# Optimization experiments

Hardware: AMD Instinct MI355X
Metric: run time of the kernel (lower is better)

## Reference

```python
import jax, jax.numpy as jnp
import numpy as np

N = 100000
E = 600000
D = 128
H = 8
DH = D // H
T = 32
NET = 2


def _ln(x, g, b, eps=1e-5):
    mu = jnp.mean(x, axis=-1, keepdims=True)
    var = jnp.mean((x - mu) ** 2, axis=-1, keepdims=True)
    return (x - mu) * jax.lax.rsqrt(var + eps) * g + b


def _expmap(e, c):
    abs_c = jnp.maximum(jnp.abs(c), 1e-15)
    sq = jnp.sqrt(abs_c)
    n = jnp.maximum(jnp.linalg.norm(e, axis=-1, keepdims=True), 1e-15)
    tanh_p = jnp.tanh(sq * n) * e / (sq * n)
    tan_p = jnp.tan(sq * n) * e / (sq * n)
    return jnp.where(c < 0, tanh_p, tan_p)


def _proj(x, c, eps=1e-5):
    abs_c = jnp.maximum(jnp.abs(c), 1e-15)
    maxnorm = (1.0 - eps) / jnp.sqrt(abs_c)
    norm = jnp.linalg.norm(x, axis=-1, keepdims=True)
    scale = jnp.where(norm > maxnorm, maxnorm / norm, jnp.ones_like(norm))
    return x * scale


def _forward(x, time_emb, edge_time, Wq, Wk, Wv, rel_q, rel_k, rel_v, Wt, bt,
             Wd1, bd1, Wd2, bd2, decay_scale, c_mag, hyp_beta, logit_alpha,
             Wo, bo, g1, be1, g2, be2, Wf1, bf1, Wf2, bf2, src, dst, edge_type):
    n = x.shape[0]
    Q = (x @ Wq).reshape(n, H, DH)
    K = (x @ Wk).reshape(n, H, DH)
    V = (x @ Wv).reshape(n, H, DH)
    # per-edge gathers + relation embeddings
    q_dst = Q[dst] + rel_q[edge_type].reshape(-1, H, DH)
    k_src = K[src] + rel_k[edge_type].reshape(-1, H, DH)
    v_src = V[src] + rel_v[edge_type].reshape(-1, H, DH)
    k_src = k_src + (time_emb @ Wt + bt).reshape(-1, H, DH)
    euclid = jnp.sum(q_dst * k_src, axis=-1) / np.float32(np.sqrt(DH))  # (E,H)
    # decay MLP: input = [edge_time, normalized edge_type]
    denom_t = jnp.maximum(1.0, edge_type.max().astype(jnp.float32) + 1.0)
    et = edge_type.astype(jnp.float32)[:, None] / denom_t
    dec_in = jnp.concatenate([edge_time[:, None], et], axis=-1)  # (E,2)
    decay_raw = jnp.tanh(jax.nn.relu(dec_in @ Wd1 + bd1) @ Wd2 + bd2)  # (E,H)
    decay = jnp.exp(decay_scale[None, :] * decay_raw)
    euclid = euclid * decay
    # hyperbolic branch
    c = -jnp.abs(c_mag)
    m = _proj(_expmap(x, c), c)
    man_dist = jnp.linalg.norm(m[src] - m[dst], axis=-1)[:, None]  # (E,1)
    hyp = -hyp_beta[None, :] * man_dist * decay
    alpha = jax.nn.sigmoid(logit_alpha)[None, :]
    logits = alpha * euclid + (1.0 - alpha) * hyp  # (E,H)
    # scatter softmax over incoming edges of each dst node
    seg_max = jax.ops.segment_max(logits, dst, num_segments=n)
    ex = jnp.exp(logits - seg_max[dst])
    denom = jax.ops.segment_sum(ex, dst, num_segments=n)
    attn = ex / denom[dst]
    agg = jax.ops.segment_sum(v_src * attn[..., None], dst, num_segments=n).reshape(n, D)
    out = agg @ Wo + bo
    x = _ln(x + out, g1, be1)
    ffn = jax.nn.gelu(x @ Wf1 + bf1, approximate=False) @ Wf2 + bf2
    x = _ln(x + ffn, g2, be2)
    return x


def setup_inputs() -> dict:
    key = jax.random.key(0)
    ks = jax.random.split(key, 20)

    def lin(k, fi, fo):
        return jax.random.normal(k, (fi, fo), jnp.float32) / np.float32(np.sqrt(fi))

    return {
        "x": jax.random.normal(ks[0], (N, D), jnp.float32),
        "edge_index": jax.random.randint(ks[1], (2, E), 0, N),
        "time_emb": jax.random.normal(ks[2], (E, T), jnp.float32),
        "edge_type": jax.random.randint(ks[3], (E,), 0, NET),
        "edge_time": jax.random.uniform(ks[4], (E,), jnp.float32),
        "Wq": lin(ks[5], D, D), "Wk": lin(ks[6], D, D), "Wv": lin(ks[7], D, D),
        "rel_q": jax.random.normal(ks[8], (NET, D), jnp.float32) * 0.1,
        "rel_k": jax.random.normal(ks[9], (NET, D), jnp.float32) * 0.1,
        "rel_v": jax.random.normal(ks[10], (NET, D), jnp.float32) * 0.1,
        "Wt": lin(ks[11], T, D), "bt": jnp.zeros((D,), jnp.float32),
        "Wd1": lin(ks[12], 2, 64), "bd1": jnp.zeros((64,), jnp.float32),
        "Wd2": lin(ks[13], 64, H), "bd2": jnp.zeros((H,), jnp.float32),
        "decay_scale": jnp.full((H,), 0.5, jnp.float32),
        "c_mag": jnp.asarray(1.0, jnp.float32),
        "hyp_beta": jnp.ones((H,), jnp.float32),
        "logit_alpha": jnp.zeros((H,), jnp.float32),
        "Wo": lin(ks[14], D, D), "bo": jnp.zeros((D,), jnp.float32),
        "g1": jnp.ones((D,), jnp.float32), "be1": jnp.zeros((D,), jnp.float32),
        "g2": jnp.ones((D,), jnp.float32), "be2": jnp.zeros((D,), jnp.float32),
        "Wf1": lin(ks[15], D, 4 * D), "bf1": jnp.zeros((4 * D,), jnp.float32),
        "Wf2": lin(ks[16], 4 * D, D), "bf2": jnp.zeros((D,), jnp.float32),
    }


def reference(x, edge_index, time_emb, edge_type, edge_time, Wq, Wk, Wv,
              rel_q, rel_k, rel_v, Wt, bt, Wd1, bd1, Wd2, bd2, decay_scale,
              c_mag, hyp_beta, logit_alpha, Wo, bo, g1, be1, g2, be2,
              Wf1, bf1, Wf2, bf2):
    src, dst = edge_index[0], edge_index[1]
    return _forward(x, time_emb, edge_time, Wq, Wk, Wv, rel_q, rel_k, rel_v,
                    Wt, bt, Wd1, bd1, Wd2, bd2, decay_scale, c_mag, hyp_beta,
                    logit_alpha, Wo, bo, g1, be1, g2, be2, Wf1, bf1, Wf2, bf2,
                    src, dst, edge_type)
```

## Files before the change

kernel.cpp:

```cpp
#include <hip/hip_runtime.h>

constexpr int NN = 100000;
constexpr int EE = 600000;
constexpr int DD = 128;
constexpr int HH = 8;
constexpr int NB = (NN + 255) / 256;

constexpr long long OFF_Q    = 0;
constexpr long long OFF_K    = OFF_Q    + (long long)NN*DD;
constexpr long long OFF_V    = OFF_K    + (long long)NN*DD;
constexpr long long OFF_LOG  = OFF_V    + (long long)NN*DD;
constexpr long long OFF_T    = OFF_LOG  + (long long)EE*HH;
constexpr long long OFF_U    = OFF_T    + (long long)NN;
constexpr long long OFF_ETM  = OFF_U    + (long long)NN;
constexpr long long OFF_CNT  = OFF_ETM  + 4;
constexpr long long OFF_CUR  = OFF_CNT  + (long long)NN;
constexpr long long OFF_RP   = OFF_CUR  + (long long)NN;
constexpr long long OFF_ES   = OFF_RP   + (long long)NN + 4;
constexpr long long OFF_SRCS = OFF_ES   + (long long)EE;
constexpr long long OFF_DSTS = OFF_SRCS + (long long)EE;
constexpr long long OFF_ETS  = OFF_DSTS + (long long)EE;
constexpr long long OFF_BS   = OFF_ETS  + (long long)EE;

typedef float f32x4 __attribute__((ext_vector_type(4)));
typedef short s16x8 __attribute__((ext_vector_type(8)));

__device__ inline float gelu_exact(float v) {
    return 0.5f * v * (1.0f + erff(v * 0.70710678118654752440f));
}
__device__ inline void bsplit1(float x, unsigned short& hb, unsigned short& lb) {
    unsigned u = __float_as_uint(x);
    hb = (unsigned short)(u >> 16);
    float rem = x - __uint_as_float(((unsigned)hb) << 16);
    lb = (unsigned short)(__float_as_uint(rem) >> 16);
}

__global__ __launch_bounds__(256) void k_zero(int* __restrict__ cnt, int* __restrict__ cur,
                                              int* __restrict__ etmax) {
    int stride = gridDim.x * 256;
    for (int i = blockIdx.x * 256 + threadIdx.x; i < NN; i += stride) { cnt[i] = 0; cur[i] = 0; }
    if (blockIdx.x == 0 && threadIdx.x == 0) etmax[0] = 0;
}

__global__ __launch_bounds__(256) void k_etmax(const int* __restrict__ etype, int* __restrict__ etmax) {
    int lmax = 0;
    int stride = gridDim.x * 256;
    for (int i = blockIdx.x * 256 + threadIdx.x; i < EE; i += stride) lmax = max(lmax, etype[i]);
    for (int m = 1; m < 64; m <<= 1) lmax = max(lmax, __shfl_xor(lmax, m));
    if ((threadIdx.x & 63) == 0) atomicMax(etmax, lmax);
}

__global__ __launch_bounds__(256) void k_hist(const int* __restrict__ eidx, int* __restrict__ cnt) {
    int i = blockIdx.x * 256 + threadIdx.x;
    if (i < EE) atomicAdd(&cnt[eidx[EE + i]], 1);
}
__global__ __launch_bounds__(256) void k_scan1(const int* __restrict__ cnt, int* __restrict__ bs) {
    __shared__ int wsum[4];
    int i = blockIdx.x * 256 + threadIdx.x;
    int v = (i < NN) ? cnt[i] : 0;
    for (int m = 1; m < 64; m <<= 1) v += __shfl_xor(v, m);
    if ((threadIdx.x & 63) == 0) wsum[threadIdx.x >> 6] = v;
    __syncthreads();
    if (threadIdx.x == 0) bs[blockIdx.x] = wsum[0] + wsum[1] + wsum[2] + wsum[3];
}
__global__ __launch_bounds__(512) void k_scan2(int* __restrict__ bs) {
    __shared__ int s[512];
    int t = threadIdx.x;
    int v = (t < NB) ? bs[t] : 0;
    s[t] = v;
    __syncthreads();
    for (int off = 1; off < 512; off <<= 1) {
        int val = 0;
        if (t >= off) val = s[t - off];
        __syncthreads();
        if (t >= off) s[t] += val;
        __syncthreads();
    }
    if (t < NB) bs[t] = s[t] - v;
}
__global__ __launch_bounds__(256) void k_scan3(const int* __restrict__ cnt, const int* __restrict__ bs,
                                               int* __restrict__ rp) {
    __shared__ int s[256];
    int t = threadIdx.x;
    int i = blockIdx.x * 256 + t;
    int v = (i < NN) ? cnt[i] : 0;
    s[t] = v;
    __syncthreads();
    for (int off = 1; off < 256; off <<= 1) {
        int val = 0;
        if (t >= off) val = s[t - off];
        __syncthreads();
        if (t >= off) s[t] += val;
        __syncthreads();
    }
    int incl = s[t];
    int off0 = bs[blockIdx.x];
    if (i < NN) rp[i] = off0 + incl - v;
    if (i == NN - 1) rp[NN] = off0 + incl;
}
__global__ __launch_bounds__(256) void k_scatter(const int* __restrict__ eidx, const int* __restrict__ etype,
                                                 const int* __restrict__ rp, int* __restrict__ cur,
                                                 int* __restrict__ es, int* __restrict__ src_s,
                                                 int* __restrict__ dst_s, int* __restrict__ et_s) {
    int i = blockIdx.x * 256 + threadIdx.x;
    if (i < EE) {
        int d = eidx[EE + i];
        int pos = rp[d] + atomicAdd(&cur[d], 1);
        es[pos] = i;
        src_s[pos] = eidx[i];
        dst_s[pos] = d;
        et_s[pos] = etype[i];
    }
}

__global__ __launch_bounds__(256) void k_qkv(const float* __restrict__ x,
                                             const float* __restrict__ Wq, const float* __restrict__ Wk,
                                             const float* __restrict__ Wv,
                                             float* __restrict__ Q, float* __restrict__ K, float* __restrict__ V) {
    __shared__ float Ast[32][72];
    __shared__ float Bs[32][72];
    int tid = threadIdx.x;
    int nt = blockIdx.y;
    int mat = nt >> 1;
    int colbase = (nt & 1) * 64;
    const float* W = (mat == 0) ? Wq : (mat == 1) ? Wk : Wv;
    float* Out = (mat == 0) ? Q : (mat == 1) ? K : V;
    int row0 = blockIdx.x * 64;
    int tx = tid & 15, ty = tid >> 4;
    float acc[4][4] = {};
    for (int k0 = 0; k0 < 128; k0 += 32) {
        {
            int r = tid >> 3;
            int c = (tid & 7) * 4;
            #pragma unroll
            for (int rr = 0; rr < 2; ++rr) {
                int lrow = r + rr * 32;
                int grow = row0 + lrow;
                float4 v = make_float4(0.f, 0.f, 0.f, 0.f);
                if (grow < NN) v = *(const float4*)&x[(long long)grow * 128 + k0 + c];
                Ast[c + 0][lrow] = v.x; Ast[c + 1][lrow] = v.y;
                Ast[c + 2][lrow] = v.z; Ast[c + 3][lrow] = v.w;
            }
            int kk = tid >> 4;
            int cc = (tid & 15) * 4;
            #pragma unroll
            for (int k2 = 0; k2 < 2; ++k2) {
                int kr = kk + k2 * 16;
                *(float4*)&Bs[kr][cc] = *(const float4*)&W[(k0 + kr) * 128 + colbase + cc];
            }
        }
        __syncthreads();
        #pragma unroll
        for (int kk = 0; kk < 32; ++kk) {
            float4 a = *(const float4*)&Ast[kk][ty * 4];
            float4 b = *(const float4*)&Bs[kk][tx * 4];
            float av[4] = {a.x, a.y, a.z, a.w};
            float bv[4] = {b.x, b.y, b.z, b.w};
            #pragma unroll
            for (int i = 0; i < 4; ++i)
                #pragma unroll
                for (int j = 0; j < 4; ++j) acc[i][j] += av[i] * bv[j];
        }
        __syncthreads();
    }
    #pragma unroll
    for (int i = 0; i < 4; ++i) {
        int grow = row0 + ty * 4 + i;
        if (grow < NN)
            *(float4*)&Out[(long long)grow * 128 + colbase + tx * 4] =
                make_float4(acc[i][0], acc[i][1], acc[i][2], acc[i][3]);
    }
}

__global__ __launch_bounds__(256) void k_tu(const float* __restrict__ x, const float* __restrict__ c_mag,
                                            float* __restrict__ T, float* __restrict__ U) {
    int wid = threadIdx.x >> 6;
    int lane = threadIdx.x & 63;
    int row = blockIdx.x * 4 + wid;
    if (row >= NN) return;
    float c = -fabsf(c_mag[0]);
    float abs_c = fmaxf(fabsf(c), 1e-15f);
    float sq = sqrtf(abs_c);
    float2 xv = *(const float2*)&x[(long long)row * 128 + lane * 2];
    float s = xv.x * xv.x + xv.y * xv.y;
    for (int m = 1; m < 64; m <<= 1) s += __shfl_xor(s, m);
    float nt = sqrtf(s);
    float n = fmaxf(nt, 1e-15f);
    float arg = sq * n;
    float f = ((c < 0.0f) ? tanhf(arg) : tanf(arg)) / arg;
    float norm = fabsf(f) * nt;
    float maxnorm = (1.0f - 1e-5f) / sq;
    float scale = (norm > maxnorm) ? (maxnorm / norm) : 1.0f;
    float t = f * scale;
    if (lane == 0) { T[row] = t; U[row] = t * t * s; }
}

__global__ __launch_bounds__(256) void k_logits(const float* __restrict__ Q, const float* __restrict__ K,
                                                const float* __restrict__ x, const float* __restrict__ T,
                                                const float* __restrict__ U, const float* __restrict__ temb,
                                                const int* __restrict__ es, const int* __restrict__ src_s,
                                                const int* __restrict__ dst_s, const int* __restrict__ et_s,
                                                const float* __restrict__ etime,
                                                const float* __restrict__ rel_q, const float* __restrict__ rel_k,
                                                const float* __restrict__ Wt, const float* __restrict__ bt,
                                                const float* __restrict__ Wd1, const float* __restrict__ bd1,
                                                const float* __restrict__ Wd2, const float* __restrict__ bd2,
                                                const float* __restrict__ dscale, const int* __restrict__ etmax,
                                                const float* __restrict__ hyp_beta,
                                                const float* __restrict__ logit_alpha,
                                                float* __restrict__ LOG) {
    __shared__ float Ts[32][32];
    __shared__ float TP[32][128];
    __shared__ float Dec[32][8];
    __shared__ float Wd1s[128];
    __shared__ float bd1s[64];
    __shared__ float Wd2s[512];
    int tid = threadIdx.x;
    int pb0 = blockIdx.x * 32;
    {
        int er = tid >> 3;
        int c = (tid & 7) * 4;
        int e = es[pb0 + er];
        *(float4*)&Ts[er][c] = *(const float4*)&temb[(long long)e * 32 + c];
        if (tid < 128) Wd1s[tid] = Wd1[tid];
        if (tid >= 128 && tid < 192) bd1s[tid - 128] = bd1[tid - 128];
        Wd2s[tid] = Wd2[tid];
        Wd2s[tid + 256] = Wd2[tid + 256];
    }
    __syncthreads();
    {
        int el = tid >> 3, hh = tid & 7;
        int pos = pb0 + el;
        float denom_t = fmaxf(1.0f, (float)(etmax[0]) + 1.0f);
        float in0 = etime[es[pos]];
        float in1 = (float)et_s[pos] / denom_t;
        float acc = bd2[hh];
        #pragma unroll
        for (int j = 0; j < 64; ++j) {
            float hid = fmaxf(in0 * Wd1s[j] + in1 * Wd1s[64 + j] + bd1s[j], 0.0f);
            acc += hid * Wd2s[j * 8 + hh];
        }
        Dec[el][hh] = expf(dscale[hh] * tanhf(acc));
    }
    {
        int c4 = (tid & 31) * 4;
        int g = tid >> 5;
        float4 bt4 = *(const float4*)&bt[c4];
        float4 a0 = bt4, a1 = bt4, a2 = bt4, a3 = bt4;
        for (int t = 0; t < 32; ++t) {
            float4 w = *(const float4*)&Wt[t * 128 + c4];
            float f0 = Ts[g][t], f1 = Ts[g + 8][t], f2 = Ts[g + 16][t], f3 = Ts[g + 24][t];
            a0.x += f0 * w.x; a0.y += f0 * w.y; a0.z += f0 * w.z; a0.w += f0 * w.w;
            a1.x += f1 * w.x; a1.y += f1 * w.y; a1.z += f1 * w.z; a1.w += f1 * w.w;
            a2.x += f2 * w.x; a2.y += f2 * w.y; a2.z += f2 * w.z; a2.w += f2 * w.w;
            a3.x += f3 * w.x; a3.y += f3 * w.y; a3.z += f3 * w.z; a3.w += f3 * w.w;
        }
        *(float4*)&TP[g][c4] = a0;
        *(float4*)&TP[g + 8][c4] = a1;
        *(float4*)&TP[g + 16][c4] = a2;
        *(float4*)&TP[g + 24][c4] = a3;
    }
    __syncthreads();
    int wid = tid >> 6;
    int lane = tid & 63;
    int half = lane >> 5;
    int l = lane & 31;
    int d4 = l * 4;
    int h = l >> 2;
    float alpha = 1.0f / (1.0f + expf(-logit_alpha[h]));
    float beta = hyp_beta[h];
    #pragma unroll
    for (int i = 0; i < 4; ++i) {
        int elocal = wid * 8 + i * 2 + half;
        int pos = pb0 + elocal;
        int src = src_s[pos], dst = dst_s[pos];
        int et = et_s[pos];
        float4 q  = *(const float4*)&Q[(long long)dst * 128 + d4];
        float4 rq = *(const float4*)&rel_q[et * 128 + d4];
        float4 k  = *(const float4*)&K[(long long)src * 128 + d4];
        float4 rk = *(const float4*)&rel_k[et * 128 + d4];
        float4 tp = *(const float4*)&TP[elocal][d4];
        float4 xs = *(const float4*)&x[(long long)src * 128 + d4];
        float4 xd = *(const float4*)&x[(long long)dst * 128 + d4];
        float ep = (q.x + rq.x) * (k.x + rk.x + tp.x)
                 + (q.y + rq.y) * (k.y + rk.y + tp.y)
                 + (q.z + rq.z) * (k.z + rk.z + tp.z)
                 + (q.w + rq.w) * (k.w + rk.w + tp.w);
        float dp = xs.x * xd.x + xs.y * xd.y + xs.z * xd.z + xs.w * xd.w;
        ep += __shfl_xor(ep, 1); ep += __shfl_xor(ep, 2);
        dp += __shfl_xor(dp, 1); dp += __shfl_xor(dp, 2); dp += __shfl_xor(dp, 4);
        dp += __shfl_xor(dp, 8); dp += __shfl_xor(dp, 16);
        float man2 = fmaxf(U[src] + U[dst] - 2.0f * T[src] * T[dst] * dp, 0.0f);
        float man = sqrtf(man2);
        float dec = Dec[elocal][h];
        float eu = ep * 0.25f * dec;
        float hyp = -beta * man * dec;
        float lg = alpha * eu + (1.0f - alpha) * hyp;
        if ((l & 3) == 0) LOG[(long long)pos * 8 + h] = lg;
    }
}

__global__ __launch_bounds__(256) void k_agg2(const int* __restrict__ rp, const int* __restrict__ src_s,
                                              const int* __restrict__ et_s,
                                              const float* __restrict__ V, const float* __restrict__ rel_v,
                                              const float* __restrict__ LOG, float* __restrict__ AGG) {
    int wid = threadIdx.x >> 6, lane = threadIdx.x & 63;
    int node = blockIdx.x * 4 + wid;
    if (node >= NN) return;
    int beg = rp[node], end = rp[node + 1];
    int d = lane * 2;
    int h = lane >> 3;
    float mx = -3.0e38f;
    for (int i = beg; i < end; ++i) {
        mx = fmaxf(mx, LOG[(long long)i * 8 + h]);
    }
    float den = 0.0f;
    float ax = 0.0f, ay = 0.0f;
    for (int i = beg; i < end; ++i) {
        int src = src_s[i];
        int et = et_s[i];
        float ex = expf(LOG[(long long)i * 8 + h] - mx);
        den += ex;
        float2 v  = *(const float2*)&V[(long long)src * 128 + d];
        float2 rv = *(const float2*)&rel_v[et * 128 + d];
        ax += (v.x + rv.x) * ex;
        ay += (v.y + rv.y) * ex;
    }
    float sc = (end > beg) ? (1.0f / den) : 0.0f;
    *(float2*)&AGG[(long long)node * 128 + d] = make_float2(ax * sc, ay * sc);
}

__global__ __launch_bounds__(256) void k_cvt(const float* __restrict__ Wf1, const float* __restrict__ Wf2,
                                             unsigned short* __restrict__ W1h, unsigned short* __restrict__ W1l,
                                             unsigned short* __restrict__ W2h, unsigned short* __restrict__ W2l) {
    int idx = blockIdx.x * 256 + threadIdx.x;
    {
        int tile = idx >> 11, rem = idx & 2047;
        int ks = rem >> 9, rem2 = rem & 511;
        int l = rem2 >> 3, j = rem2 & 7;
        int k = ks * 32 + ((l >> 4) << 3) + j;
        int n = (tile << 4) + (l & 15);
        unsigned short hb, lb;
        bsplit1(Wf1[k * 512 + n], hb, lb);
        W1h[idx] = hb; W1l[idx] = lb;
    }
    {
        int tile = idx >> 13;
        int ks = (idx >> 9) & 15;
        int l = (idx >> 3) & 63, j = idx & 7;
        int k = ks * 32 + ((l >> 4) << 3) + j;
        int n = (tile << 4) + (l & 15);
        unsigned short hb, lb;
        bsplit1(Wf2[k * 128 + n], hb, lb);
        W2h[idx] = hb; W2l[idx] = lb;
    }
}

__global__ __launch_bounds__(256) void k_out_ln1(float* AGGY1,
                                                 const float* __restrict__ Wo,
                                                 const float* __restrict__ bo, const float* __restrict__ x,
                                                 const float* __restrict__ g1, const float* __restrict__ be1) {
    __shared__ float Ast[32][40];
    __shared__ float Bs[32][136];
    int tid = threadIdx.x;
    int row0 = blockIdx.x * 32;
    int tx = tid & 31, ty = tid >> 5;
    float acc[4][4] = {};
    for (int k0 = 0; k0 < 128; k0 += 32) {
        {
            int r = tid >> 3, c = (tid & 7) * 4;
            float4 v = *(const float4*)&AGGY1[(long long)(row0 + r) * 128 + k0 + c];
            Ast[c + 0][r] = v.x; Ast[c + 1][r] = v.y; Ast[c + 2][r] = v.z; Ast[c + 3][r] = v.w;
            int kk = tid >> 5, cc = (tid & 31) * 4;
            #pragma unroll
            for (int k2 = 0; k2 < 4; ++k2) {
                int kr = kk + k2 * 8;
                *(float4*)&Bs[kr][cc] = *(const float4*)&Wo[(k0 + kr) * 128 + cc];
            }
        }
        __syncthreads();
        #pragma unroll
        for (int kk = 0; kk < 32; ++kk) {
            float4 a = *(const float4*)&Ast[kk][ty * 4];
            float4 b = *(const float4*)&Bs[kk][tx * 4];
            float av[4] = {a.x, a.y, a.z, a.w};
            float bv[4] = {b.x, b.y, b.z, b.w};
            #pragma unroll
            for (int i = 0; i < 4; ++i)
                #pragma unroll
                for (int j = 0; j < 4; ++j) acc[i][j] += av[i] * bv[j];
        }
        __syncthreads();
    }
    float4 bov = *(const float4*)&bo[tx * 4];
    float4 g = *(const float4*)&g1[tx * 4];
    float4 bb = *(const float4*)&be1[tx * 4];
    #pragma unroll
    for (int i = 0; i < 4; ++i) {
        int row = row0 + ty * 4 + i;
        float4 xv = *(const float4*)&x[(long long)row * 128 + tx * 4];
        float v0 = xv.x + acc[i][0] + bov.x;
        float v1 = xv.y + acc[i][1] + bov.y;
        float v2 = xv.z + acc[i][2] + bov.z;
        float v3 = xv.w + acc[i][3] + bov.w;
        float sum = v0 + v1 + v2 + v3;
        for (int m = 1; m < 32; m <<= 1) sum += __shfl_xor(sum, m);
        float mu = sum * (1.0f / 128.0f);
        float d0 = v0 - mu, d1 = v1 - mu, d2 = v2 - mu, d3 = v3 - mu;
        float ss = d0 * d0 + d1 * d1 + d2 * d2 + d3 * d3;
        for (int m = 1; m < 32; m <<= 1) ss += __shfl_xor(ss, m);
        float var = ss * (1.0f / 128.0f);
        float rs = 1.0f / sqrtf(var + 1e-5f);
        float4 o;
        o.x = d0 * rs * g.x + bb.x;
        o.y = d1 * rs * g.y + bb.y;
        o.z = d2 * rs * g.z + bb.z;
        o.w = d3 * rs * g.w + bb.w;
        *(float4*)&AGGY1[(long long)row * 128 + tx * 4] = o;
    }
}

__global__ __launch_bounds__(256) void k_ffn_ln2(float* IO,
        const unsigned short* __restrict__ W1h, const unsigned short* __restrict__ W1l,
        const unsigned short* __restrict__ W2h, const unsigned short* __restrict__ W2l,
        const float* __restrict__ bf1, const float* __restrict__ bf2,
        const float* __restrict__ g2, const float* __restrict__ be2) {
    __shared__ __align__(16) float Ys[16][132];
    __shared__ __align__(16) short Yfrag[2][2048];
    __shared__ __align__(16) float Hs[16][516];
    __shared__ __align__(16) short Hfrag[2][4096];
    int tid = threadIdx.x;
    int row0 = blockIdx.x * 16;
    int wave = tid >> 6, l = tid & 63;
    {
        int r = tid >> 4, c = (tid & 15) * 8;
        float4 a = *(const float4*)&IO[(long long)(row0 + r) * 128 + c];
        float4 b = *(const float4*)&IO[(long long)(row0 + r) * 128 + c + 4];
        *(float4*)&Ys[r][c] = a;
        *(float4*)&Ys[r][c + 4] = b;
    }
    __syncthreads();
    {
        int ks = tid >> 6, ll = tid & 63;
        int rr = ll & 15, kb = ks * 32 + ((ll >> 4) << 3);
        float4 p0 = *(const float4*)&Ys[rr][kb];
        float4 p1 = *(const float4*)&Ys[rr][kb + 4];
        float av[8] = {p0.x, p0.y, p0.z, p0.w, p1.x, p1.y, p1.z, p1.w};
        s16x8 vh, vl;
        #pragma unroll
        for (int j = 0; j < 8; ++j) {
            unsigned short hb, lb;
            bsplit1(av[j], hb, lb);
            vh[j] = (short)hb; vl[j] = (short)lb;
        }
        *(s16x8*)&Yfrag[0][(ks * 64 + ll) * 8] = vh;
        *(s16x8*)&Yfrag[1][(ks * 64 + ll) * 8] = vl;
    }
    __syncthreads();
    {
        f32x4 zero = {0.0f, 0.0f, 0.0f, 0.0f};
        f32x4 acc[8];
        #pragma unroll
        for (int t = 0; t < 8; ++t) acc[t] = zero;
        #pragma unroll
        for (int ks = 0; ks < 4; ++ks) {
            s16x8 ah = *(const s16x8*)&Yfrag[0][(ks * 64 + l) * 8];
            s16x8 al = *(const s16x8*)&Yfrag[1][(ks * 64 + l) * 8];
            #pragma unroll
            for (int t = 0; t < 8; ++t) {
                int idx = (((wave * 8 + t) * 4 + ks) * 64 + l) * 8;
                s16x8 bh = *(const s16x8*)&W1h[idx];
                s16x8 bl = *(const s16x8*)&W1l[idx];
                acc[t] = __builtin_amdgcn_mfma_f32_16x16x32_bf16(ah, bh, acc[t], 0, 0, 0);
                acc[t] = __builtin_amdgcn_mfma_f32_16x16x32_bf16(ah, bl, acc[t], 0, 0, 0);
                acc[t] = __builtin_amdgcn_mfma_f32_16x16x32_bf16(al, bh, acc[t], 0, 0, 0);
            }
        }
        int rb = (l >> 4) * 4, cl = l & 15;
        #pragma unroll
        for (int t = 0; t < 8; ++t) {
            int col = (wave * 8 + t) * 16 + cl;
            float bb = bf1[col];
            #pragma unroll
            for (int r = 0; r < 4; ++r)
                Hs[rb + r][col] = gelu_exact(acc[t][r] + bb);
        }
    }
    __syncthreads();
    f32x4 acc2[2];
    acc2[0] = (f32x4){0.0f, 0.0f, 0.0f, 0.0f};
    acc2[1] = (f32x4){0.0f, 0.0f, 0.0f, 0.0f};
    #pragma unroll
    for (int halfk = 0; halfk < 2; ++halfk) {
        {
            int ksh = tid >> 5, lg = tid & 31;
            #pragma unroll
            for (int q = 0; q < 2; ++q) {
                int l2 = lg * 2 + q;
                int rr = l2 & 15, kb = (halfk * 8 + ksh) * 32 + ((l2 >> 4) << 3);
                float4 p0 = *(const float4*)&Hs[rr][kb];
                float4 p1 = *(const float4*)&Hs[rr][kb + 4];
                float av[8] = {p0.x, p0.y, p0.z, p0.w, p1.x, p1.y, p1.z, p1.w};
                s16x8 vh, vl;
                #pragma unroll
                for (int j = 0; j < 8; ++j) {
                    unsigned short hb, lb;
                    bsplit1(av[j], hb, lb);
                    vh[j] = (short)hb; vl[j] = (short)lb;
                }
                *(s16x8*)&Hfrag[0][(ksh * 64 + l2) * 8] = vh;
                *(s16x8*)&Hfrag[1][(ksh * 64 + l2) * 8] = vl;
            }
        }
        __syncthreads();
        #pragma unroll
        for (int ksl = 0; ksl < 8; ++ksl) {
            int ks = halfk * 8 + ksl;
            s16x8 ah = *(const s16x8*)&Hfrag[0][(ksl * 64 + l) * 8];
            s16x8 al = *(const s16x8*)&Hfrag[1][(ksl * 64 + l) * 8];
            #pragma unroll
            for (int t = 0; t < 2; ++t) {
                int idx = (((wave * 2 + t) * 16 + ks) * 64 + l) * 8;
                s16x8 bh = *(const s16x8*)&W2h[idx];
                s16x8 bl = *(const s16x8*)&W2l[idx];
                acc2[t] = __builtin_amdgcn_mfma_f32_16x16x32_bf16(ah, bh, acc2[t], 0, 0, 0);
                acc2[t] = __builtin_amdgcn_mfma_f32_16x16x32_bf16(ah, bl, acc2[t], 0, 0, 0);
                acc2[t] = __builtin_amdgcn_mfma_f32_16x16x32_bf16(al, bh, acc2[t], 0, 0, 0);
            }
        }
        __syncthreads();
    }
    float* Os = (float*)&Yfrag[0][0];
    {
        int rb = (l >> 4) * 4, cl = l & 15;
        #pragma unroll
        for (int t = 0; t < 2; ++t) {
            int col = (wave * 2 + t) * 16 + cl;
            #pragma unroll
            for (int r = 0; r < 4; ++r)
                Os[(rb + r) * 128 + col] = acc2[t][r];
        }
    }
    __syncthreads();
    {
        int cg = (tid & 31) * 4;
        int rp_ = (tid >> 5) * 2;
        float4 b2 = *(const float4*)&bf2[cg];
        float4 g = *(const float4*)&g2[cg];
        float4 bb = *(const float4*)&be2[cg];
        #pragma unroll
        for (int r = 0; r < 2; ++r) {
            int rr = rp_ + r;
            int row = row0 + rr;
            float v0 = Ys[rr][cg + 0] + Os[rr * 128 + cg + 0] + b2.x;
            float v1 = Ys[rr][cg + 1] + Os[rr * 128 + cg + 1] + b2.y;
            float v2 = Ys[rr][cg + 2] + Os[rr * 128 + cg + 2] + b2.z;
            float v3 = Ys[rr][cg + 3] + Os[rr * 128 + cg + 3] + b2.w;
            float sum = v0 + v1 + v2 + v3;
            for (int m = 1; m < 32; m <<= 1) sum += __shfl_xor(sum, m);
            float mu = sum * (1.0f / 128.0f);
            float d0 = v0 - mu, d1 = v1 - mu, d2 = v2 - mu, d3 = v3 - mu;
            float ss = d0 * d0 + d1 * d1 + d2 * d2 + d3 * d3;
            for (int m = 1; m < 32; m <<= 1) ss += __shfl_xor(ss, m);
            float var = ss * (1.0f / 128.0f);
            float rs = 1.0f / sqrtf(var + 1e-5f);
            float4 o;
            o.x = d0 * rs * g.x + bb.x;
            o.y = d1 * rs * g.y + bb.y;
            o.z = d2 * rs * g.z + bb.z;
            o.w = d3 * rs * g.w + bb.w;
            *(float4*)&IO[(long long)row * 128 + cg] = o;
        }
    }
}

extern "C" void kernel_launch(void* const* d_in, const int* in_sizes, int n_in,
                              void* d_out, int out_size, void* d_ws, size_t ws_size,
                              hipStream_t stream) {
    const float* x       = (const float*)d_in[0];
    const int*   eidx    = (const int*)d_in[1];
    const float* temb    = (const float*)d_in[2];
    const int*   etype   = (const int*)d_in[3];
    const float* etime   = (const float*)d_in[4];
    const float* Wq      = (const float*)d_in[5];
    const float* Wk      = (const float*)d_in[6];
    const float* Wv      = (const float*)d_in[7];
    const float* rel_q   = (const float*)d_in[8];
    const float* rel_k   = (const float*)d_in[9];
    const float* rel_v   = (const float*)d_in[10];
    const float* Wt      = (const float*)d_in[11];
    const float* bt      = (const float*)d_in[12];
    const float* Wd1     = (const float*)d_in[13];
    const float* bd1     = (const float*)d_in[14];
    const float* Wd2     = (const float*)d_in[15];
    const float* bd2     = (const float*)d_in[16];
    const float* dscale  = (const float*)d_in[17];
    const float* c_mag   = (const float*)d_in[18];
    const float* hbeta   = (const float*)d_in[19];
    const float* lalpha  = (const float*)d_in[20];
    const float* Wo      = (const float*)d_in[21];
    const float* bo      = (const float*)d_in[22];
    const float* g1      = (const float*)d_in[23];
    const float* be1     = (const float*)d_in[24];
    const float* g2      = (const float*)d_in[25];
    const float* be2     = (const float*)d_in[26];
    const float* Wf1     = (const float*)d_in[27];
    const float* bf1     = (const float*)d_in[28];
    const float* Wf2     = (const float*)d_in[29];
    const float* bf2     = (const float*)d_in[30];

    float* ws = (float*)d_ws;
    float*    Q    = ws + OFF_Q;
    float*    K    = ws + OFF_K;
    float*    V    = ws + OFF_V;
    float*    LOG  = ws + OFF_LOG;
    float*    T    = ws + OFF_T;
    float*    U    = ws + OFF_U;
    int*      ETM  = (int*)(ws + OFF_ETM);
    int*      CNT  = (int*)(ws + OFF_CNT);
    int*      CUR  = (int*)(ws + OFF_CUR);
    int*      RP   = (int*)(ws + OFF_RP);
    int*      ES   = (int*)(ws + OFF_ES);
    int*      SRCS = (int*)(ws + OFF_SRCS);
    int*      DSTS = (int*)(ws + OFF_DSTS);
    int*      ETS  = (int*)(ws + OFF_ETS);
    int*      BS   = (int*)(ws + OFF_BS);
    float*    AGG  = (float*)d_out;
    float*    IO   = (float*)d_out;
    unsigned short* W1h = (unsigned short*)(ws + OFF_V);
    unsigned short* W1l = W1h + 65536;
    unsigned short* W2h = W1l + 65536;
    unsigned short* W2l = W2h + 65536;

    k_zero<<<512, 256, 0, stream>>>(CNT, CUR, ETM);
    k_etmax<<<512, 256, 0, stream>>>(etype, ETM);
    k_hist<<<(EE + 255) / 256, 256, 0, stream>>>(eidx, CNT);
    k_scan1<<<NB, 256, 0, stream>>>(CNT, BS);
    k_scan2<<<1, 512, 0, stream>>>(BS);
    k_scan3<<<NB, 256, 0, stream>>>(CNT, BS, RP);
    k_scatter<<<(EE + 255) / 256, 256, 0, stream>>>(eidx, etype, RP, CUR, ES, SRCS, DSTS, ETS);
    k_qkv<<<dim3(1563, 6), 256, 0, stream>>>(x, Wq, Wk, Wv, Q, K, V);
    k_tu<<<25000, 256, 0, stream>>>(x, c_mag, T, U);
    k_logits<<<EE / 32, 256, 0, stream>>>(Q, K, x, T, U, temb, ES, SRCS, DSTS, ETS, etime,
                                          rel_q, rel_k, Wt, bt, Wd1, bd1, Wd2, bd2,
                                          dscale, ETM, hbeta, lalpha, LOG);
    k_agg2<<<25000, 256, 0, stream>>>(RP, SRCS, ETS, V, rel_v, LOG, AGG);
    k_cvt<<<256, 256, 0, stream>>>(Wf1, Wf2, W1h, W1l, W2h, W2l);
    k_out_ln1<<<NN / 32, 256, 0, stream>>>(AGG, Wo, bo, x, g1, be1);
    k_ffn_ln2<<<NN / 16, 256, 0, stream>>>(IO, W1h, W1l, W2h, W2l, bf1, bf2, g2, be2);
}
```

Before: 1.073 ms.

## Use split-bf16 MFMA for QKV projection and time-embedding projection

Replaces the scalar FP32 tiled GEMM for Q/K/V and the per-edge time-embedding projection with bf16x3 (hi/lo split) MFMA 16x16x32 instructions. A new pre-kernel converts Wq/Wk/Wv/Wt into hi/lo bf16 fragments laid out in MFMA operand order. The aim is to move these matmuls onto matrix cores while keeping near-FP32 accuracy. It adds one small conversion kernel and extra workspace, and writes outputs with scalar stores instead of float4.

```diff
diff --git a/kernel.cpp b/kernel.cpp
--- a/kernel.cpp
+++ b/kernel.cpp
@@ -21,6 +21,8 @@
 constexpr long long OFF_DSTS = OFF_SRCS + (long long)EE;
 constexpr long long OFF_ETS  = OFF_DSTS + (long long)EE;
 constexpr long long OFF_BS   = OFF_ETS  + (long long)EE;
+constexpr long long OFF_WQKVF= OFF_BS   + 512;
+constexpr long long OFF_WTF  = OFF_WQKVF+ 49152;
 
 typedef float f32x4 __attribute__((ext_vector_type(4)));
 typedef short s16x8 __attribute__((ext_vector_type(8)));
@@ -113,62 +115,91 @@
     }
 }
 
+__global__ __launch_bounds__(256) void k_cvt_pre(const float* __restrict__ Wq, const float* __restrict__ Wk,
+                                                 const float* __restrict__ Wv, const float* __restrict__ Wt,
+                                                 unsigned short* __restrict__ WQKVh, unsigned short* __restrict__ WQKVl,
+                                                 unsigned short* __restrict__ WTh, unsigned short* __restrict__ WTl) {
+    int idx = blockIdx.x * 256 + threadIdx.x;
+    if (idx < 49152) {
+        int mat = idx >> 14, r = idx & 16383;
+        int tile = r >> 11, ks = (r >> 9) & 3, l = (r >> 3) & 63, j = r & 7;
+        int k = ks * 32 + ((l >> 4) << 3) + j;
+        int n = (tile << 4) + (l & 15);
+        const float* W = (mat == 0) ? Wq : (mat == 1) ? Wk : Wv;
+        unsigned short hb, lb;
+        bsplit1(W[k * 128 + n], hb, lb);
+        WQKVh[idx] = hb; WQKVl[idx] = lb;
+    } else {
+        int r = idx - 49152;
+        int tile = r >> 9, l = (r >> 3) & 63, j = r & 7;
+        int k = ((l >> 4) << 3) + j;
+        int n = (tile << 4) + (l & 15);
+        unsigned short hb, lb;
+        bsplit1(Wt[k * 128 + n], hb, lb);
+        WTh[r] = hb; WTl[r] = lb;
+    }
+}
+
 __global__ __launch_bounds__(256) void k_qkv(const float* __restrict__ x,
-                                             const float* __restrict__ Wq, const float* __restrict__ Wk,
-                                             const float* __restrict__ Wv,
+                                             const unsigned short* __restrict__ WQKVh,
+                                             const unsigned short* __restrict__ WQKVl,
                                              float* __restrict__ Q, float* __restrict__ K, float* __restrict__ V) {
-    __shared__ float Ast[32][72];
-    __shared__ float Bs[32][72];
+    __shared__ __align__(16) short Xfrag[2][8192];
     int tid = threadIdx.x;
-    int nt = blockIdx.y;
-    int mat = nt >> 1;
-    int colbase = (nt & 1) * 64;
-    const float* W = (mat == 0) ? Wq : (mat == 1) ? Wk : Wv;
+    int wave = tid >> 6, l = tid & 63;
+    int mat = blockIdx.y;
     float* Out = (mat == 0) ? Q : (mat == 1) ? K : V;
     int row0 = blockIdx.x * 64;
-    int tx = tid & 15, ty = tid >> 4;
-    float acc[4][4] = {};
-    for (int k0 = 0; k0 < 128; k0 += 32) {
-        {
-            int r = tid >> 3;
-            int c = (tid & 7) * 4;
-            #pragma unroll
-            for (int rr = 0; rr < 2; ++rr) {
-                int lrow = r + rr * 32;
-                int grow = row0 + lrow;
-                float4 v = make_float4(0.f, 0.f, 0.f, 0.f);
-                if (grow < NN) v = *(const float4*)&x[(long long)grow * 128 + k0 + c];
-                Ast[c + 0][lrow] = v.x; Ast[c + 1][lrow] = v.y;
-                Ast[c + 2][lrow] = v.z; Ast[c + 3][lrow] = v.w;
-            }
-            int kk = tid >> 4;
-            int cc = (tid & 15) * 4;
-            #pragma unroll
-            for (int k2 = 0; k2 < 2; ++k2) {
-                int kr = kk + k2 * 16;
-                *(float4*)&Bs[kr][cc] = *(const float4*)&W[(k0 + kr) * 128 + colbase + cc];
-            }
-        }
-        __syncthreads();
-        #pragma unroll
-        for (int kk = 0; kk < 32; ++kk) {
-            float4 a = *(const float4*)&Ast[kk][ty * 4];
-            float4 b = *(const float4*)&Bs[kk][tx * 4];
-            float av[4] = {a.x, a.y, a.z, a.w};
-            float bv[4] = {b.x, b.y, b.z, b.w};
-            #pragma unroll
-            for (int i = 0; i < 4; ++i)
-                #pragma unroll
-                for (int j = 0; j < 4; ++j) acc[i][j] += av[i] * bv[j];
-        }
-        __syncthreads();
-    }
     #pragma unroll
-    for (int i = 0; i < 4; ++i) {
-        int grow = row0 + ty * 4 + i;
-        if (grow < NN)
-            *(float4*)&Out[(long long)grow * 128 + colbase + tx * 4] =
-                make_float4(acc[i][0], acc[i][1], acc[i][2], acc[i][3]);
+    for (int it = 0; it < 4; ++it) {
+        int pair = it * 4 + wave;
+        int rg = pair >> 2, ks = pair & 3;
+        int grow = row0 + rg * 16 + (l & 15);
+        int kb = ks * 32 + ((l >> 4) << 3);
+        float4 p0 = make_float4(0.f, 0.f, 0.f, 0.f), p1 = make_float4(0.f, 0.f, 0.f, 0.f);
+        if (grow < NN) {
+            p0 = *(const float4*)&x[(long long)grow * 128 + kb];
+            p1 = *(const float4*)&x[(long long)grow * 128 + kb + 4];
+        }
+        float av[8] = {p0.x, p0.y, p0.z, p0.w, p1.x, p1.y, p1.z, p1.w};
+        s16x8 vh, vl;
+        #pragma unroll
+        for (int j = 0; j < 8; ++j) {
+            unsigned short hb, lb;
+            bsplit1(av[j], hb, lb);
+            vh[j] = (short)hb; vl[j] = (short)lb;
+        }
+        *(s16x8*)&Xfrag[0][(pair * 64 + l) * 8] = vh;
+        *(s16x8*)&Xfrag[1][(pair * 64 + l) * 8] = vl;
+    }
+    __syncthreads();
+    f32x4 acc[8];
+    #pragma unroll
+    for (int t = 0; t < 8; ++t) acc[t] = (f32x4){0.f, 0.f, 0.f, 0.f};
+    #pragma unroll
+    for (int ks = 0; ks < 4; ++ks) {
+        s16x8 ah = *(const s16x8*)&Xfrag[0][((wave * 4 + ks) * 64 + l) * 8];
+        s16x8 al = *(const s16x8*)&Xfrag[1][((wave * 4 + ks) * 64 + l) * 8];
+        #pragma unroll
+        for (int t = 0; t < 8; ++t) {
+            int bidx = mat * 16384 + (t * 4 + ks) * 512 + l * 8;
+            s16x8 bh = *(const s16x8*)&WQKVh[bidx];
+            s16x8 bl = *(const s16x8*)&WQKVl[bidx];
+            acc[t] = __builtin_amdgcn_mfma_f32_16x16x32_bf16(ah, bh, acc[t], 0, 0, 0);
+            acc[t] = __builtin_amdgcn_mfma_f32_16x16x32_bf16(ah, bl, acc[t], 0, 0, 0);
+            acc[t] = __builtin_amdgcn_mfma_f32_16x16x32_bf16(al, bh, acc[t], 0, 0, 0);
+        }
+    }
+    int rb = row0 + wave * 16 + ((l >> 4) << 2);
+    int cl = l & 15;
+    #pragma unroll
+    for (int t = 0; t < 8; ++t) {
+        int col = t * 16 + cl;
+        #pragma unroll
+        for (int r = 0; r < 4; ++r) {
+            int row = rb + r;
+            if (row < NN) Out[(long long)row * 128 + col] = acc[t][r];
+        }
     }
 }
 
@@ -202,7 +233,9 @@
                                                 const int* __restrict__ dst_s, const int* __restrict__ et_s,
                                                 const float* __restrict__ etime,
                                                 const float* __restrict__ rel_q, const float* __restrict__ rel_k,
-                                                const float* __restrict__ Wt, const float* __restrict__ bt,
+                                                const unsigned short* __restrict__ WTh,
+                                                const unsigned short* __restrict__ WTl,
+                                                const float* __restrict__ bt,
                                                 const float* __restrict__ Wd1, const float* __restrict__ bd1,
                                                 const float* __restrict__ Wd2, const float* __restrict__ bd2,
                                                 const float* __restrict__ dscale, const int* __restrict__ etmax,
@@ -216,6 +249,7 @@
     __shared__ float bd1s[64];
     __shared__ float Wd2s[512];
     int tid = threadIdx.x;
+    int wave = tid >> 6, l = tid & 63;
     int pb0 = blockIdx.x * 32;
     {
         int er = tid >> 3;
@@ -243,30 +277,44 @@
         Dec[el][hh] = expf(dscale[hh] * tanhf(acc));
     }
     {
-        int c4 = (tid & 31) * 4;
-        int g = tid >> 5;
-        float4 bt4 = *(const float4*)&bt[c4];
-        float4 a0 = bt4, a1 = bt4, a2 = bt4, a3 = bt4;
-        for (int t = 0; t < 32; ++t) {
-            float4 w = *(const float4*)&Wt[t * 128 + c4];
-            float f0 = Ts[g][t], f1 = Ts[g + 8][t], f2 = Ts[g + 16][t], f3 = Ts[g + 24][t];
-            a0.x += f0 * w.x; a0.y += f0 * w.y; a0.z += f0 * w.z; a0.w += f0 * w.w;
-            a1.x += f1 * w.x; a1.y += f1 * w.y; a1.z += f1 * w.z; a1.w += f1 * w.w;
-            a2.x += f2 * w.x; a2.y += f2 * w.y; a2.z += f2 * w.z; a2.w += f2 * w.w;
-            a3.x += f3 * w.x; a3.y += f3 * w.y; a3.z += f3 * w.z; a3.w += f3 * w.w;
-        }
-        *(float4*)&TP[g][c4] = a0;
-        *(float4*)&TP[g + 8][c4] = a1;
-        *(float4*)&TP[g + 16][c4] = a2;
-        *(float4*)&TP[g + 24][c4] = a3;
-    }
-    __syncthreads();
-    int wid = tid >> 6;
-    int lane = tid & 63;
+        int eg = wave >> 1;
+        int tb = (wave & 1) * 4;
+        int kb = (l >> 4) << 3;
+        float4 p0 = *(const float4*)&Ts[eg * 16 + (l & 15)][kb];
+        float4 p1 = *(const float4*)&Ts[eg * 16 + (l & 15)][kb + 4];
+        float av[8] = {p0.x, p0.y, p0.z, p0.w, p1.x, p1.y, p1.z, p1.w};
+        s16x8 ah, al;
+        #pragma unroll
+        for (int j = 0; j < 8; ++j) {
+            unsigned short hb, lb;
+            bsplit1(av[j], hb, lb);
+            ah[j] = (short)hb; al[j] = (short)lb;
+        }
+        int rbl = eg * 16 + ((l >> 4) << 2);
+        #pragma unroll
+        for (int t = 0; t < 4; ++t) {
+            int tile = tb + t;
+            int bidx = tile * 512 + l * 8;
+            s16x8 bh = *(const s16x8*)&WTh[bidx];
+            s16x8 bl = *(const s16x8*)&WTl[bidx];
+            f32x4 acc = (f32x4){0.f, 0.f, 0.f, 0.f};
+            acc = __builtin_amdgcn_mfma_f32_16x16x32_bf16(ah, bh, acc, 0, 0, 0);
+            acc = __builtin_amdgcn_mfma_f32_16x16x32_bf16(ah, bl, acc, 0, 0, 0);
+            acc = __builtin_amdgcn_mfma_f32_16x16x32_bf16(al, bh, acc, 0, 0, 0);
+            int col = tile * 16 + (l & 15);
+            float btv = bt[col];
+            #pragma unroll
+            for (int r = 0; r < 4; ++r)
+                TP[rbl + r][col] = acc[r] + btv;
+        }
+    }
+    __syncthreads();
+    int wid = wave;
+    int lane = l;
     int half = lane >> 5;
-    int l = lane & 31;
-    int d4 = l * 4;
-    int h = l >> 2;
+    int ll = lane & 31;
+    int d4 = ll * 4;
+    int h = ll >> 2;
     float alpha = 1.0f / (1.0f + expf(-logit_alpha[h]));
     float beta = hyp_beta[h];
     #pragma unroll
@@ -296,7 +344,7 @@
         float eu = ep * 0.25f * dec;
         float hyp = -beta * man * dec;
         float lg = alpha * eu + (1.0f - alpha) * hyp;
-        if ((l & 3) == 0) LOG[(long long)pos * 8 + h] = lg;
+        if ((ll & 3) == 0) LOG[(long long)pos * 8 + h] = lg;
     }
 }
 
@@ -625,6 +673,10 @@
     int*      DSTS = (int*)(ws + OFF_DSTS);
     int*      ETS  = (int*)(ws + OFF_ETS);
     int*      BS   = (int*)(ws + OFF_BS);
+    unsigned short* WQKVh = (unsigned short*)(ws + OFF_WQKVF);
+    unsigned short* WQKVl = WQKVh + 49152;
+    unsigned short* WTh   = (unsigned short*)(ws + OFF_WTF);
+    unsigned short* WTl   = WTh + 4096;
     float*    AGG  = (float*)d_out;
     float*    IO   = (float*)d_out;
     unsigned short* W1h = (unsigned short*)(ws + OFF_V);
@@ -633,16 +685,17 @@
     unsigned short* W2l = W2h + 65536;
 
     k_zero<<<512, 256, 0, stream>>>(CNT, CUR, ETM);
+    k_cvt_pre<<<208, 256, 0, stream>>>(Wq, Wk, Wv, Wt, WQKVh, WQKVl, WTh, WTl);
     k_etmax<<<512, 256, 0, stream>>>(etype, ETM);
     k_hist<<<(EE + 255) / 256, 256, 0, stream>>>(eidx, CNT);
     k_scan1<<<NB, 256, 0, stream>>>(CNT, BS);
     k_scan2<<<1, 512, 0, stream>>>(BS);
     k_scan3<<<NB, 256, 0, stream>>>(CNT, BS, RP);
     k_scatter<<<(EE + 255) / 256, 256, 0, stream>>>(eidx, etype, RP, CUR, ES, SRCS, DSTS, ETS);
-    k_qkv<<<dim3(1563, 6), 256, 0, stream>>>(x, Wq, Wk, Wv, Q, K, V);
+    k_qkv<<<dim3(1563, 3), 256, 0, stream>>>(x, WQKVh, WQKVl, Q, K, V);
     k_tu<<<25000, 256, 0, stream>>>(x, c_mag, T, U);
     k_logits<<<EE / 32, 256, 0, stream>>>(Q, K, x, T, U, temb, ES, SRCS, DSTS, ETS, etime,
-                                          rel_q, rel_k, Wt, bt, Wd1, bd1, Wd2, bd2,
+                                          rel_q, rel_k, WTh, WTl, bt, Wd1, bd1, Wd2, bd2,
                                           dscale, ETM, hbeta, lalpha, LOG);
     k_agg2<<<25000, 256, 0, stream>>>(RP, SRCS, ETS, V, rel_v, LOG, AGG);
     k_cvt<<<256, 256, 0, stream>>>(Wf1, Wf2, W1h, W1l, W2h, W2l);
```

New measurement: 987.6 us. 7.9% less time.
